# Kernel tuning notes

Measured on AMD Instinct MI355X. Metric: run time of the kernel, lower is better.

Reference implementation:

```python
import jax, jax.numpy as jnp
import numpy as np
from jax import lax

B, CIN, H, W = 8, 64, 128, 128
COUT, K, STRIDE, PAD = 128, 3, 1, 1
NLEV = 256  # 2**activation_bits == 2**weight_bits


def setup_inputs() -> dict:
    key = jax.random.key(0)
    kx, kw = jax.random.split(key)
    x = jax.random.uniform(kx, (B, CIN, H, W), dtype=jnp.float32)
    weight = jax.random.normal(kw, (COUT, CIN, K, K), dtype=jnp.float32)
    bias = jnp.zeros((COUT,), dtype=jnp.float32)
    return {"x": x, "weight": weight, "bias": bias}


def _lut_table(weight):
    # quantized weights in [0, 255], integer-valued
    qw = jnp.clip(jnp.round(weight * (NLEV - 1)), 0, NLEV - 1).astype(jnp.int32)
    iv = jnp.arange(NLEV, dtype=jnp.int32)
    # emulate torch .to(int16) wraparound (qw*i can exceed 32767)
    lut = (qw[..., None] * iv).astype(jnp.int16)          # [O, C, K, K, 256]
    # the original sums pcilt over its (c,p,q) dims for EVERY patch entry;
    # precollapse those dims: T[i, o] = sum_{c,p,q} lut[o,c,p,q,i]
    T = lut.astype(jnp.int32).sum(axis=(1, 2, 3))          # [O, 256]
    return T.T                                             # [256, O]


def reference(x, weight, bias):
    T = _lut_table(weight)                                 # [256, COUT]
    xq = jnp.clip(jnp.round(x * (NLEV - 1)), 0, NLEV - 1).astype(jnp.int32)
    xp = jnp.pad(xq, ((0, 0), (0, 0), (PAD, PAD), (PAD, PAD)))  # zero-pad; T[:,0]=0 matches
    xc = jnp.moveaxis(xp, 1, 0)                            # [CIN, B, Hp, Wp]

    # accumulate per-pixel channel sum of LUT rows: A[b,h,w,o] = sum_c T[x[b,c,h,w], o]
    A0 = jnp.zeros((xp.shape[0], xp.shape[2], xp.shape[3], COUT), dtype=jnp.int32)

    def body(acc, ch):
        return acc + T[ch], None

    A, _ = lax.scan(body, A0, xc)                          # [B, Hp, Wp, COUT]

    # k x k sliding-window sum over spatial dims = sum over all patch entries
    out = lax.reduce_window(A.astype(jnp.float32), 0.0, lax.add,
                            (1, K, K, 1), (1, STRIDE, STRIDE, 1), 'VALID')
    out = jnp.moveaxis(out, 3, 1) + bias[None, :, None, None]  # [B, COUT, OH, OW]
    return out
```

## Files before the change

kernel.cpp:

```cpp
#include <hip/hip_runtime.h>

#define CIN   64
#define HW    128
#define COUT  128
#define TH    8
#define TW    32
#define PXR   34
#define NITER (TH + 3)
#define NTHR  512
#define HSTR  144
#define AKSTR 136

typedef int v4i __attribute__((ext_vector_type(4)));

__device__ __forceinline__ void wg_barrier() {
  asm volatile("s_waitcnt lgkmcnt(0)\n\ts_barrier" ::: "memory");
}

__global__ __launch_bounds__(128)
void build_tables(const float* __restrict__ weight, int* __restrict__ W_tab,
                  char* __restrict__ Kt_g) {
  __shared__ int qw_s[576];
  __shared__ int red_s[128];
  const int o = blockIdx.x;
  const int t = threadIdx.x;
  int partial = 0;
  for (int j = t; j < 576; j += 128) {
    float w = weight[o * 576 + j];
    int q = (int)rintf(w * 255.f);
    q = q < 0 ? 0 : (q > 255 ? 255 : q);
    qw_s[j] = q;
    partial += q;
  }
  red_s[t] = partial;
  __syncthreads();
  for (int s = 64; s > 0; s >>= 1) {
    if (t < s) red_s[t] += red_s[t + s];
    __syncthreads();
  }
  if (t == 0) W_tab[o] = red_s[0];
  const int i = 128 + t;
  int cnt = 0;
  for (int j = 0; j < 576; ++j) cnt += (qw_s[j] * i) > 32767 ? 1 : 0;
  Kt_g[o * 128 + t] = (char)(cnt - 128);
}

__global__ __launch_bounds__(NTHR, 4)
void pcilt_main(const float* __restrict__ x, const float* __restrict__ bias,
                const int* __restrict__ W_tab, const char* __restrict__ Kt_g,
                float* __restrict__ out) {
  __shared__ unsigned char Hm[5][48 * HSTR];
  __shared__ unsigned char Kt[16384];
  __shared__ unsigned short AK[2][48 * AKSTR];
  __shared__ int SxSH[8][40];

  const int t   = (int)threadIdx.x;
  const int bid = (int)blockIdx.x;
  const int b  = bid & 7;
  const int k  = bid >> 3;
  const int h0 = (k >> 2) * TH;
  const int w0 = (k & 3) * TW;

  for (int i = t; i < 4096; i += NTHR)
    ((unsigned int*)Kt)[i] = ((const unsigned int*)Kt_g)[i];
  {
    const uint4 z4 = make_uint4(0, 0, 0, 0);
    for (int i = t; i < 5 * 48 * HSTR / 16; i += NTHR) ((uint4*)Hm)[i] = z4;
    if (t < 320) ((int*)SxSH)[t] = 0;
  }

  const int l    = t & 15;
  const int slot = t >> 4;
  const int w    = t >> 6;
  const int kq   = (t >> 4) & 3;
  const int we   = t & 31;
  const int og   = t >> 5;

  float wf[8], bi[8];
#pragma unroll
  for (int m = 0; m < 8; ++m) {
    wf[m] = (float)W_tab[og * 8 + m];
    bi[m] = bias[og * 8 + m];
  }

  wg_barrier();

  v4i bfr[4][2];
  const int Mt = w >> 1, Nh = w & 1;
  if (w < 6) {
#pragma unroll
    for (int nt = 0; nt < 4; ++nt)
#pragma unroll
      for (int k64 = 0; k64 < 2; ++k64)
        bfr[nt][k64] = *(const v4i*)(Kt + (Nh * 64 + nt * 16 + l) * 128 +
                                     k64 * 64 + kq * 16);
  }

  float pf0[4], pf1[4];
  const float* xb = x + ((size_t)b * CIN + l * 4) * (HW * HW);
  const size_t cs = (size_t)HW * HW;

#define ISSUE(rn)                                                              \
  {                                                                            \
    const int iy  = h0 + (rn)-1;                                               \
    const int iyc = iy < 0 ? 0 : (iy > 127 ? 127 : iy);                        \
    const bool rok = (iy >= 0) && (iy < HW);                                   \
    int ix = w0 + slot - 1;                                                    \
    int ixc = ix < 0 ? 0 : (ix > 127 ? 127 : ix);                              \
    bool ok = rok && (ix >= 0) && (ix < HW);                                   \
    const float* xp = xb + (size_t)iyc * HW + ixc;                             \
    float v0 = xp[0], v1 = xp[cs], v2 = xp[2 * cs], v3 = xp[3 * cs];           \
    pf0[0] = ok ? v0 : 0.f; pf0[1] = ok ? v1 : 0.f;                            \
    pf0[2] = ok ? v2 : 0.f; pf0[3] = ok ? v3 : 0.f;                            \
    if (slot < 2) {                                                            \
      ix = w0 + 32 + slot - 1;                                                 \
      ixc = ix > 127 ? 127 : ix;                                               \
      ok = rok && (ix < HW);                                                   \
      const float* xq = xb + (size_t)iyc * HW + ixc;                           \
      float u0 = xq[0], u1 = xq[cs], u2 = xq[2 * cs], u3 = xq[3 * cs];         \
      pf1[0] = ok ? u0 : 0.f; pf1[1] = ok ? u1 : 0.f;                          \
      pf1[2] = ok ? u2 : 0.f; pf1[3] = ok ? u3 : 0.f;                          \
    }                                                                          \
  }

#define STAGEPX(pf, px)                                                        \
  {                                                                            \
    int q, iv0, iv1, iv2, iv3;                                                 \
    q = (int)rintf((pf)[0] * 255.f); iv0 = q < 0 ? 0 : (q > 255 ? 255 : q);    \
    q = (int)rintf((pf)[1] * 255.f); iv1 = q < 0 ? 0 : (q > 255 ? 255 : q);    \
    q = (int)rintf((pf)[2] * 255.f); iv2 = q < 0 ? 0 : (q > 255 ? 255 : q);    \
    q = (int)rintf((pf)[3] * 255.f); iv3 = q < 0 ? 0 : (q > 255 ? 255 : q);    \
    int ps = iv0 + iv1 + iv2 + iv3;                                            \
    int pc = (iv0 > 128) + (iv1 > 128) + (iv2 > 128) + (iv3 > 128);            \
    atomicAdd(&Sp[px], (pc << 20) + ps);                                       \
    unsigned char* hp = Hc + (px)*HSTR;                                        \
    if (iv0 > 128) { int v = iv0 - 128; atomicAdd((unsigned int*)(hp + ((v >> 2) << 2)), 1u << ((v & 3) * 8)); } \
    if (iv1 > 128) { int v = iv1 - 128; atomicAdd((unsigned int*)(hp + ((v >> 2) << 2)), 1u << ((v & 3) * 8)); } \
    if (iv2 > 128) { int v = iv2 - 128; atomicAdd((unsigned int*)(hp + ((v >> 2) << 2)), 1u << ((v & 3) * 8)); } \
    if (iv3 > 128) { int v = iv3 - 128; atomicAdd((unsigned int*)(hp + ((v >> 2) << 2)), 1u << ((v & 3) * 8)); } \
  }

  ISSUE(0);

  for (int r = 0; r < NITER; ++r) {
    if (r <= TH + 1) {
      unsigned char* Hc = (unsigned char*)Hm[r % 5];
      int* Sp = SxSH[r & 7];
      STAGEPX(pf0, slot);
      if (slot < 2) STAGEPX(pf1, 32 + slot);
      if (r + 1 <= TH + 1) ISSUE(r + 1);
    }
    wg_barrier();

    if (r >= 2 && r <= TH + 1 && w < 6) {
      v4i acc[4];
#pragma unroll
      for (int nt = 0; nt < 4; ++nt) acc[nt] = (v4i){0, 0, 0, 0};
      const int prow = Mt * 16 + (t & 15);
#pragma unroll
      for (int st = 0; st < 3; ++st) {
        const unsigned char* Hs = (const unsigned char*)Hm[(r - 2 + st) % 5] +
                                  prow * HSTR + kq * 16;
#pragma unroll
        for (int k64 = 0; k64 < 2; ++k64) {
          const v4i a = *(const v4i*)(Hs + k64 * 64);
#pragma unroll
          for (int nt = 0; nt < 4; ++nt)
            acc[nt] = __builtin_amdgcn_mfma_i32_16x16x64_i8(a, bfr[nt][k64], acc[nt], 0, 0, 0);
        }
      }
      unsigned short* AKw = AK[r & 1];
      const int pbase = Mt * 16 + kq * 4;
#pragma unroll
      for (int nt = 0; nt < 4; ++nt) {
        const int o = Nh * 64 + nt * 16 + (t & 15);
#pragma unroll
        for (int rg = 0; rg < 4; ++rg)
          AKw[(pbase + rg) * AKSTR + o] = (unsigned short)acc[nt][rg];
      }
    }
    if (w >= 6 && r >= 3 && r <= TH - 1) {
      const uint4 z4 = make_uint4(0, 0, 0, 0);
      uint4* Hn = (uint4*)Hm[(r + 2) % 5];
      for (int i = t - 384; i < 34 * HSTR / 16; i += 128) Hn[i] = z4;
      if (t - 384 < 40) SxSH[(r + 2) & 7][t - 384] = 0;
    }

    if (r >= 3) {
      const int h = h0 + r - 3;
      const unsigned short* AKr = AK[(r - 1) & 1];
      int v9 = 0;
#pragma unroll
      for (int q = 0; q < 3; ++q) {
        const int sl = (r - 3 + q) & 7;
        v9 += SxSH[sl][we] + SxSH[sl][we + 1] + SxSH[sl][we + 2];
      }
      const int sx9 = v9 & 0xFFFFF;
      const int sh9 = v9 >> 20;
      int k0 = 0, k1 = 0, k2 = 0, k3 = 0, k4 = 0, k5 = 0, k6 = 0, k7 = 0;
#pragma unroll
      for (int dx = 0; dx < 3; ++dx) {
        const uint4 p = *(const uint4*)&AKr[(we + dx) * AKSTR + og * 8];
        k0 += (int)(short)(p.x & 0xffffu); k1 += (int)(short)(p.x >> 16);
        k2 += (int)(short)(p.y & 0xffffu); k3 += (int)(short)(p.y >> 16);
        k4 += (int)(short)(p.z & 0xffffu); k5 += (int)(short)(p.z >> 16);
        k6 += (int)(short)(p.w & 0xffffu); k7 += (int)(short)(p.w >> 16);
      }
      const int kc = 128 * sh9;
      const float sxf = (float)sx9;
      float* op = out + (((size_t)b * COUT + og * 8) * HW + h) * HW + (w0 + we);
      const size_t os = (size_t)HW * HW;
      op[0 * os] = sxf * wf[0] - 65536.f * (float)(k0 + kc) + bi[0];
      op[1 * os] = sxf * wf[1] - 65536.f * (float)(k1 + kc) + bi[1];
      op[2 * os] = sxf * wf[2] - 65536.f * (float)(k2 + kc) + bi[2];
      op[3 * os] = sxf * wf[3] - 65536.f * (float)(k3 + kc) + bi[3];
      op[4 * os] = sxf * wf[4] - 65536.f * (float)(k4 + kc) + bi[4];
      op[5 * os] = sxf * wf[5] - 65536.f * (float)(k5 + kc) + bi[5];
      op[6 * os] = sxf * wf[6] - 65536.f * (float)(k6 + kc) + bi[6];
      op[7 * os] = sxf * wf[7] - 65536.f * (float)(k7 + kc) + bi[7];
    }
  }
}

extern "C" void kernel_launch(void* const* d_in, const int* in_sizes, int n_in,
                              void* d_out, int out_size, void* d_ws, size_t ws_size,
                              hipStream_t stream) {
  const float* x      = (const float*)d_in[0];
  const float* weight = (const float*)d_in[1];
  const float* bias   = (const float*)d_in[2];
  float* out = (float*)d_out;

  int*  W_tab = (int*)d_ws;
  char* Kt_g  = (char*)d_ws + 512;

  build_tables<<<128, 128, 0, stream>>>(weight, W_tab, Kt_g);

  pcilt_main<<<512, NTHR, 0, stream>>>(x, bias, W_tab, Kt_g, out);
}
```

Baseline: 46.52 us.

## Shrink LDS footprint with 4-slot ring and aliased AK buffer for higher occupancy

```diff
diff --git a/kernel.cpp b/kernel.cpp
--- a/kernel.cpp
+++ b/kernel.cpp
@@ -6,10 +6,16 @@
 #define TH    8
 #define TW    32
 #define PXR   34
-#define NITER (TH + 3)
+#define NITER (TH + 2)
 #define NTHR  512
 #define HSTR  144
 #define AKSTR 136
+#define SLOT  (PXR * HSTR)
+
+#define LDS_BYTES 36608
+#define HM_OFF    0
+#define KT_OFF    19584
+#define SX_OFF    35968
 
 typedef int v4i __attribute__((ext_vector_type(4)));
 
@@ -45,14 +51,16 @@
   Kt_g[o * 128 + t] = (char)(cnt - 128);
 }
 
-__global__ __launch_bounds__(NTHR, 4)
+__global__ __launch_bounds__(NTHR, 8)
 void pcilt_main(const float* __restrict__ x, const float* __restrict__ bias,
                 const int* __restrict__ W_tab, const char* __restrict__ Kt_g,
                 float* __restrict__ out) {
-  __shared__ unsigned char Hm[5][48 * HSTR];
-  __shared__ unsigned char Kt[16384];
-  __shared__ unsigned short AK[2][48 * AKSTR];
-  __shared__ int SxSH[8][40];
+  __shared__ uint4 ldsv[LDS_BYTES / 16];
+  char* ldsb = (char*)ldsv;
+  unsigned char* HmB  = (unsigned char*)(ldsb + HM_OFF);
+  unsigned char* KtB  = (unsigned char*)(ldsb + KT_OFF);
+  unsigned short* AK  = (unsigned short*)(ldsb + KT_OFF);
+  int* SxSH           = (int*)(ldsb + SX_OFF);
 
   const int t   = (int)threadIdx.x;
   const int bid = (int)blockIdx.x;
@@ -62,11 +70,11 @@
   const int w0 = (k & 3) * TW;
 
   for (int i = t; i < 4096; i += NTHR)
-    ((unsigned int*)Kt)[i] = ((const unsigned int*)Kt_g)[i];
+    ((unsigned int*)KtB)[i] = ((const unsigned int*)Kt_g)[i];
   {
     const uint4 z4 = make_uint4(0, 0, 0, 0);
-    for (int i = t; i < 5 * 48 * HSTR / 16; i += NTHR) ((uint4*)Hm)[i] = z4;
-    if (t < 320) ((int*)SxSH)[t] = 0;
+    for (int i = t; i < 4 * SLOT / 16; i += NTHR) ((uint4*)HmB)[i] = z4;
+    if (t < 160) SxSH[t] = 0;
   }
 
   const int l    = t & 15;
@@ -92,7 +100,7 @@
     for (int nt = 0; nt < 4; ++nt)
 #pragma unroll
       for (int k64 = 0; k64 < 2; ++k64)
-        bfr[nt][k64] = *(const v4i*)(Kt + (Nh * 64 + nt * 16 + l) * 128 +
+        bfr[nt][k64] = *(const v4i*)(KtB + (Nh * 64 + nt * 16 + l) * 128 +
                                      k64 * 64 + kq * 16);
   }
 
@@ -143,23 +151,23 @@
   ISSUE(0);
 
   for (int r = 0; r < NITER; ++r) {
-    if (r <= TH + 1) {
-      unsigned char* Hc = (unsigned char*)Hm[r % 5];
-      int* Sp = SxSH[r & 7];
+    {
+      unsigned char* Hc = HmB + (r & 3) * SLOT;
+      int* Sp = &SxSH[(r & 3) * 40];
       STAGEPX(pf0, slot);
       if (slot < 2) STAGEPX(pf1, 32 + slot);
-      if (r + 1 <= TH + 1) ISSUE(r + 1);
+      if (r + 1 < NITER) ISSUE(r + 1);
     }
     wg_barrier();
 
-    if (r >= 2 && r <= TH + 1 && w < 6) {
+    if (r >= 2 && w < 6) {
       v4i acc[4];
 #pragma unroll
       for (int nt = 0; nt < 4; ++nt) acc[nt] = (v4i){0, 0, 0, 0};
-      const int prow = Mt * 16 + (t & 15);
+      const int prow = Mt * 16 + l;
 #pragma unroll
       for (int st = 0; st < 3; ++st) {
-        const unsigned char* Hs = (const unsigned char*)Hm[(r - 2 + st) % 5] +
+        const unsigned char* Hs = HmB + ((r - 2 + st) & 3) * SLOT +
                                   prow * HSTR + kq * 16;
 #pragma unroll
         for (int k64 = 0; k64 < 2; ++k64) {
@@ -169,38 +177,37 @@
             acc[nt] = __builtin_amdgcn_mfma_i32_16x16x64_i8(a, bfr[nt][k64], acc[nt], 0, 0, 0);
         }
       }
-      unsigned short* AKw = AK[r & 1];
       const int pbase = Mt * 16 + kq * 4;
 #pragma unroll
       for (int nt = 0; nt < 4; ++nt) {
-        const int o = Nh * 64 + nt * 16 + (t & 15);
+        const int o = Nh * 64 + nt * 16 + l;
 #pragma unroll
         for (int rg = 0; rg < 4; ++rg)
-          AKw[(pbase + rg) * AKSTR + o] = (unsigned short)acc[nt][rg];
-      }
-    }
-    if (w >= 6 && r >= 3 && r <= TH - 1) {
+          AK[(pbase + rg) * AKSTR + o] = (unsigned short)acc[nt][rg];
+      }
+    }
+    if (w >= 6) {
       const uint4 z4 = make_uint4(0, 0, 0, 0);
-      uint4* Hn = (uint4*)Hm[(r + 2) % 5];
-      for (int i = t - 384; i < 34 * HSTR / 16; i += 128) Hn[i] = z4;
-      if (t - 384 < 40) SxSH[(r + 2) & 7][t - 384] = 0;
-    }
-
-    if (r >= 3) {
-      const int h = h0 + r - 3;
-      const unsigned short* AKr = AK[(r - 1) & 1];
+      uint4* Hn = (uint4*)(HmB + ((r + 1) & 3) * SLOT);
+      for (int i = t - 384; i < SLOT / 16; i += 128) Hn[i] = z4;
+      if (t - 384 < 40) SxSH[((r + 1) & 3) * 40 + (t - 384)] = 0;
+    }
+    wg_barrier();
+
+    if (r >= 2) {
+      const int h = h0 + r - 2;
       int v9 = 0;
 #pragma unroll
       for (int q = 0; q < 3; ++q) {
-        const int sl = (r - 3 + q) & 7;
-        v9 += SxSH[sl][we] + SxSH[sl][we + 1] + SxSH[sl][we + 2];
+        const int sl = (r - 2 + q) & 3;
+        v9 += SxSH[sl * 40 + we] + SxSH[sl * 40 + we + 1] + SxSH[sl * 40 + we + 2];
       }
       const int sx9 = v9 & 0xFFFFF;
       const int sh9 = v9 >> 20;
       int k0 = 0, k1 = 0, k2 = 0, k3 = 0, k4 = 0, k5 = 0, k6 = 0, k7 = 0;
 #pragma unroll
       for (int dx = 0; dx < 3; ++dx) {
-        const uint4 p = *(const uint4*)&AKr[(we + dx) * AKSTR + og * 8];
+        const uint4 p = *(const uint4*)&AK[(we + dx) * AKSTR + og * 8];
         k0 += (int)(short)(p.x & 0xffffu); k1 += (int)(short)(p.x >> 16);
         k2 += (int)(short)(p.y & 0xffffu); k3 += (int)(short)(p.y >> 16);
         k4 += (int)(short)(p.z & 0xffffu); k5 += (int)(short)(p.z >> 16);
```

New measurement: 130.1 us. +179.7%, slower.
